# Kernel tuning notes

Measured on AMD Instinct MI355X. Metric: run time of the kernel, lower is better.

Reference implementation:

```python
import jax, jax.numpy as jnp
import numpy as np
from jax import lax

C = 64
EPS = 1e-6

def ln2d(x, w, b):
    # channel-wise LN over HxW per (n, c)
    mean = x.mean(axis=(2, 3), keepdims=True)
    var = ((x - mean) ** 2).mean(axis=(2, 3), keepdims=True)
    return (x - mean) / jnp.sqrt(var + EPS) * w + b

def pw(x, w, b):
    # 1x1 conv: w [O, I], b [O]
    return jnp.einsum('nihw,oi->nohw', x, w) + b[None, :, None, None]

def dwconv3(x, w, b):
    # depthwise 3x3, w [2C, 1, 3, 3]
    y = lax.conv_general_dilated(x, w, window_strides=(1, 1), padding='SAME',
                                 feature_group_count=x.shape[1],
                                 dimension_numbers=('NCHW', 'OIHW', 'NCHW'))
    return y + b[None, :, None, None]

def simple_gate(x):
    x1, x2 = jnp.split(x, 2, axis=1)
    return x1 * x2

def setup_inputs() -> dict:
    key = jax.random.key(0)
    ks = jax.random.split(key, 16)
    s = 0.05
    return {
        'x': jax.random.normal(ks[0], (8, C, 256, 256), jnp.float32),
        'ln1_w': jnp.ones((1, C, 1, 1), jnp.float32),
        'ln1_b': jnp.zeros((1, C, 1, 1), jnp.float32),
        'pw1_w': jax.random.normal(ks[1], (2 * C, C), jnp.float32) * s,
        'pw1_b': jnp.zeros((2 * C,), jnp.float32),
        'dw_w': jax.random.normal(ks[2], (2 * C, 1, 3, 3), jnp.float32) * s,
        'dw_b': jnp.zeros((2 * C,), jnp.float32),
        'sca_w': jax.random.normal(ks[3], (C, C), jnp.float32) * s,
        'sca_b': jnp.zeros((C,), jnp.float32),
        'pw2_w': jax.random.normal(ks[4], (C, C), jnp.float32) * s,
        'pw2_b': jnp.zeros((C,), jnp.float32),
        'ln2_w': jnp.ones((1, C, 1, 1), jnp.float32),
        'ln2_b': jnp.zeros((1, C, 1, 1), jnp.float32),
        'pw3_w': jax.random.normal(ks[5], (2 * C, C), jnp.float32) * s,
        'pw3_b': jnp.zeros((2 * C,), jnp.float32),
        'pw4_w': jax.random.normal(ks[6], (C, C), jnp.float32) * s,
        'pw4_b': jnp.zeros((C,), jnp.float32),
        'beta1': jax.random.normal(ks[7], (1, C, 1, 1), jnp.float32) * 0.1,
        'beta2': jax.random.normal(ks[8], (1, C, 1, 1), jnp.float32) * 0.1,
    }

def reference(x, ln1_w, ln1_b, pw1_w, pw1_b, dw_w, dw_b, sca_w, sca_b,
              pw2_w, pw2_b, ln2_w, ln2_b, pw3_w, pw3_b, pw4_w, pw4_b,
              beta1, beta2):
    y = ln2d(x, ln1_w, ln1_b)
    y = pw(y, pw1_w, pw1_b)
    y = dwconv3(y, dw_w, dw_b)
    y = simple_gate(y)
    # SCA: global avg pool -> 1x1 conv -> sigmoid scale
    s = y.mean(axis=(2, 3), keepdims=True)          # [N, C, 1, 1]
    w = jax.nn.sigmoid(pw(s, sca_w, sca_b))
    y = y * w
    y = pw(y, pw2_w, pw2_b)
    x = x + beta1 * y
    y2 = ln2d(x, ln2_w, ln2_b)
    y2 = pw(y2, pw3_w, pw3_b)
    y2 = simple_gate(y2)
    y2 = pw(y2, pw4_w, pw4_b)
    return x + beta2 * y2
```

## Files before the change

kernel.cpp:

```cpp
#include <hip/hip_runtime.h>
#include <hip/hip_bf16.h>

#define NB 8
#define CC 64
#define HWP 65536

typedef __attribute__((ext_vector_type(8))) short short8;
typedef __attribute__((ext_vector_type(4))) float f32x4;

__device__ __forceinline__ short f2bf(float f) {
  union { float f; unsigned u; } v; v.f = f;
  return (short)((v.u + 0x7FFF + ((v.u >> 16) & 1)) >> 16);
}
__device__ __forceinline__ float bf2f(unsigned short u) {
  union { unsigned u; float f; } v; v.u = ((unsigned)u) << 16; return v.f;
}

__global__ __launch_bounds__(256) void ln_stats_kernel(
    const float* __restrict__ x, const float* __restrict__ lw,
    const float* __restrict__ lb, float* __restrict__ a, float* __restrict__ b) {
  int plane = blockIdx.x;
  int c = plane & 63;
  const float4* p4 = (const float4*)(x + (size_t)plane * HWP);
  float s = 0.f, s2 = 0.f;
  for (int i = threadIdx.x; i < HWP / 4; i += 256) {
    float4 v = p4[i];
    s  += v.x + v.y + v.z + v.w;
    s2 += v.x * v.x + v.y * v.y + v.z * v.z + v.w * v.w;
  }
  for (int off = 32; off; off >>= 1) {
    s  += __shfl_down(s, off);
    s2 += __shfl_down(s2, off);
  }
  __shared__ float ls[4], ls2[4];
  int wid = threadIdx.x >> 6, lid = threadIdx.x & 63;
  if (lid == 0) { ls[wid] = s; ls2[wid] = s2; }
  __syncthreads();
  if (threadIdx.x == 0) {
    float S  = ls[0] + ls[1] + ls[2] + ls[3];
    float S2 = ls2[0] + ls2[1] + ls2[2] + ls2[3];
    float mean = S * (1.f / (float)HWP);
    float var  = S2 * (1.f / (float)HWP) - mean * mean;
    float rstd = rsqrtf(var + 1e-6f);
    float av = rstd * lw[c];
    a[plane] = av;
    b[plane] = lb[c] - mean * av;
  }
}

__global__ void fold_kernel(const float* __restrict__ w, const float* __restrict__ pb,
                            const float* __restrict__ a, const float* __restrict__ b,
                            float* __restrict__ wf, float* __restrict__ cf, int O) {
  int idx = blockIdx.x * blockDim.x + threadIdx.x;
  if (idx >= NB * O) return;
  int n = idx / O, o = idx - n * O;
  const float* an = a + n * 64;
  const float* bn = b + n * 64;
  const float* wo = w + o * 64;
  float* wfo = wf + (size_t)idx * 64;
  float cc = pb[o];
  for (int i = 0; i < 64; i++) { float wv = wo[i]; wfo[i] = wv * an[i]; cc += wv * bn[i]; }
  cf[idx] = cc;
}

__global__ __launch_bounds__(256, 2) void gemm_pw1_kernel(
    const float* __restrict__ x, const float* __restrict__ wf,
    const float* __restrict__ cf, unsigned short* __restrict__ z) {
  int n = blockIdx.y;
  int lane = threadIdx.x & 63, wid = threadIdx.x >> 6;
  int col = lane & 15, quad = lane >> 4;
  short8 a[8][2];
  const float* wfn = wf + (size_t)n * 128 * 64;
  #pragma unroll
  for (int mt = 0; mt < 8; mt++)
    #pragma unroll
    for (int ks = 0; ks < 2; ks++) {
      const float* wp = wfn + (mt * 16 + col) * 64 + ks * 32 + quad * 8;
      short8 v;
      #pragma unroll
      for (int j = 0; j < 8; j++) v[j] = f2bf(wp[j]);
      a[mt][ks] = v;
    }
  float cb[8][4];
  #pragma unroll
  for (int mt = 0; mt < 8; mt++)
    #pragma unroll
    for (int r = 0; r < 4; r++) cb[mt][r] = cf[n * 128 + mt * 16 + quad * 4 + r];
  const float* xn = x + (size_t)n * 64 * HWP;
  unsigned short* zn = z + (size_t)n * 128 * HWP;
  int pxbase = blockIdx.x * 256 + wid * 16 + col;

  auto load_b = [&](int p, short8* bf) {
    #pragma unroll
    for (int ks = 0; ks < 2; ks++) {
      short8 v;
      #pragma unroll
      for (int j = 0; j < 8; j++)
        v[j] = f2bf(xn[(size_t)(ks * 32 + quad * 8 + j) * HWP + p]);
      bf[ks] = v;
    }
  };

  short8 bb[2][2];
  load_b(pxbase, bb[0]);
  #pragma unroll
  for (int tile = 0; tile < 4; tile++) {
    int cur = tile & 1, nxt = cur ^ 1;
    int p = pxbase + tile * 64;
    if (tile < 3) load_b(p + 64, bb[nxt]);
    f32x4 acc[8];
    #pragma unroll
    for (int mt = 0; mt < 8; mt++) {
      acc[mt] = (f32x4){0.f, 0.f, 0.f, 0.f};
      acc[mt] = __builtin_amdgcn_mfma_f32_16x16x32_bf16(a[mt][0], bb[cur][0], acc[mt], 0, 0, 0);
      acc[mt] = __builtin_amdgcn_mfma_f32_16x16x32_bf16(a[mt][1], bb[cur][1], acc[mt], 0, 0, 0);
    }
    #pragma unroll
    for (int mt = 0; mt < 8; mt++)
      #pragma unroll
      for (int r = 0; r < 4; r++)
        zn[(size_t)(mt * 16 + quad * 4 + r) * HWP + p] =
            (unsigned short)f2bf(acc[mt][r] + cb[mt][r]);
  }
}

__global__ __launch_bounds__(256) void dwgate_kernel(
    const unsigned short* __restrict__ z, const float* __restrict__ dww,
    const float* __restrict__ dwb, unsigned short* __restrict__ t,
    float* __restrict__ pooled2) {
  int blk = blockIdx.x;
  int plane = blk >> 1, half = blk & 1;
  int n = plane >> 6, c = plane & 63;
  int lane = threadIdx.x & 63, wv = threadIdx.x >> 6;
  const unsigned short* z0 = z + ((size_t)n * 128 + c) * HWP;
  const unsigned short* z1 = z0 + (size_t)64 * HWP;
  unsigned short* tp = t + (size_t)plane * HWP;
  float w0[9], w1[9];
  #pragma unroll
  for (int k = 0; k < 9; k++) { w0[k] = dww[c * 9 + k]; w1[k] = dww[(c + 64) * 9 + k]; }
  float bias0 = dwb[c], bias1 = dwb[c + 64];
  int r0 = half * 128 + wv * 32;
  int colb = lane * 4;

  float fa[3][4], la[3], ra[3];
  float fb[3][4], lb_[3], rb[3];

  auto loadrow = [&](const unsigned short* base, int h, float* f, float& l, float& r) {
    if ((unsigned)h < 256u) {
      ushort4 u = *(const ushort4*)(base + h * 256 + colb);
      f[0] = bf2f(u.x); f[1] = bf2f(u.y); f[2] = bf2f(u.z); f[3] = bf2f(u.w);
    } else {
      f[0] = f[1] = f[2] = f[3] = 0.f;
    }
    float ll = __shfl_up(f[3], 1);
    float rr = __shfl_down(f[0], 1);
    l = (lane == 0) ? 0.f : ll;
    r = (lane == 63) ? 0.f : rr;
  };

  loadrow(z0, r0 - 1, fa[0], la[0], ra[0]);
  loadrow(z1, r0 - 1, fb[0], lb_[0], rb[0]);
  loadrow(z0, r0,     fa[1], la[1], ra[1]);
  loadrow(z1, r0,     fb[1], lb_[1], rb[1]);

  float lsum = 0.f;
  #pragma unroll 2
  for (int h = r0; h < r0 + 32; h++) {
    loadrow(z0, h + 1, fa[2], la[2], ra[2]);
    loadrow(z1, h + 1, fb[2], lb_[2], rb[2]);
    float o0[4] = {bias0, bias0, bias0, bias0};
    float o1[4] = {bias1, bias1, bias1, bias1};
    #pragma unroll
    for (int rr_ = 0; rr_ < 3; rr_++) {
      float wl0 = w0[rr_ * 3], wc0 = w0[rr_ * 3 + 1], wr0 = w0[rr_ * 3 + 2];
      float wl1 = w1[rr_ * 3], wc1 = w1[rr_ * 3 + 1], wr1 = w1[rr_ * 3 + 2];
      const float* f0 = fa[rr_]; const float* f1 = fb[rr_];
      float l0 = la[rr_], r0h = ra[rr_], l1 = lb_[rr_], r1h = rb[rr_];
      o0[0] += wl0 * l0    + wc0 * f0[0] + wr0 * f0[1];
      o0[1] += wl0 * f0[0] + wc0 * f0[1] + wr0 * f0[2];
      o0[2] += wl0 * f0[1] + wc0 * f0[2] + wr0 * f0[3];
      o0[3] += wl0 * f0[2] + wc0 * f0[3] + wr0 * r0h;
      o1[0] += wl1 * l1    + wc1 * f1[0] + wr1 * f1[1];
      o1[1] += wl1 * f1[0] + wc1 * f1[1] + wr1 * f1[2];
      o1[2] += wl1 * f1[1] + wc1 * f1[2] + wr1 * f1[3];
      o1[3] += wl1 * f1[2] + wc1 * f1[3] + wr1 * r1h;
    }
    float g0 = o0[0] * o1[0], g1 = o0[1] * o1[1];
    float g2 = o0[2] * o1[2], g3 = o0[3] * o1[3];
    uint2 pk;
    pk.x = (unsigned)(unsigned short)f2bf(g0) | ((unsigned)(unsigned short)f2bf(g1) << 16);
    pk.y = (unsigned)(unsigned short)f2bf(g2) | ((unsigned)(unsigned short)f2bf(g3) << 16);
    *(uint2*)(tp + (size_t)h * 256 + colb) = pk;
    lsum += (g0 + g1) + (g2 + g3);
    #pragma unroll
    for (int i = 0; i < 4; i++) { fa[0][i] = fa[1][i]; fa[1][i] = fa[2][i];
                                  fb[0][i] = fb[1][i]; fb[1][i] = fb[2][i]; }
    la[0] = la[1]; la[1] = la[2]; ra[0] = ra[1]; ra[1] = ra[2];
    lb_[0] = lb_[1]; lb_[1] = lb_[2]; rb[0] = rb[1]; rb[1] = rb[2];
  }
  for (int off = 32; off; off >>= 1) lsum += __shfl_down(lsum, off);
  __shared__ float ls[4];
  if (lane == 0) ls[wv] = lsum;
  __syncthreads();
  if (threadIdx.x == 0) pooled2[plane * 2 + half] = ls[0] + ls[1] + ls[2] + ls[3];
}

__global__ void sca_kernel(const float* __restrict__ pooled2, const float* __restrict__ sw,
                           const float* __restrict__ sb, float* __restrict__ sca) {
  int idx = blockIdx.x * blockDim.x + threadIdx.x;
  if (idx >= 512) return;
  int n = idx >> 6, o = idx & 63;
  float s = sb[o];
  const float* pm = pooled2 + n * 64 * 2;
  for (int i = 0; i < 64; i++)
    s += sw[o * 64 + i] * (pm[i * 2] + pm[i * 2 + 1]) * (1.f / 65536.f);
  sca[idx] = 1.f / (1.f + expf(-s));
}

__global__ void fold_pw2_kernel(const float* __restrict__ w, const float* __restrict__ pb,
                                const float* __restrict__ sca, const float* __restrict__ beta1,
                                float* __restrict__ wf, float* __restrict__ cf) {
  int idx = blockIdx.x * blockDim.x + threadIdx.x;
  if (idx >= 512) return;
  int n = idx >> 6, o = idx & 63;
  float bt = beta1[o];
  const float* sn = sca + n * 64;
  float* wfo = wf + (size_t)idx * 64;
  for (int i = 0; i < 64; i++) wfo[i] = bt * w[o * 64 + i] * sn[i];
  cf[idx] = bt * pb[o];
}

__global__ __launch_bounds__(256, 2) void gemm_pw2_kernel(
    const unsigned short* __restrict__ t, const float* __restrict__ x,
    const float* __restrict__ wf, const float* __restrict__ cf,
    float* __restrict__ x1, float* __restrict__ part_sum, float* __restrict__ part_sq) {
  __shared__ float red_s[4][64], red_q[4][64];
  int n = blockIdx.y;
  int lane = threadIdx.x & 63, wid = threadIdx.x >> 6;
  int col = lane & 15, quad = lane >> 4;
  short8 a[4][2];
  const float* wfn = wf + (size_t)n * 64 * 64;
  #pragma unroll
  for (int mt = 0; mt < 4; mt++)
    #pragma unroll
    for (int ks = 0; ks < 2; ks++) {
      const float* wp = wfn + (mt * 16 + col) * 64 + ks * 32 + quad * 8;
      short8 v;
      #pragma unroll
      for (int j = 0; j < 8; j++) v[j] = f2bf(wp[j]);
      a[mt][ks] = v;
    }
  float cb[4][4];
  #pragma unroll
  for (int mt = 0; mt < 4; mt++)
    #pragma unroll
    for (int r = 0; r < 4; r++) cb[mt][r] = cf[n * 64 + mt * 16 + quad * 4 + r];
  const unsigned short* tn = t + (size_t)n * 64 * HWP;
  const float* xn = x + (size_t)n * 64 * HWP;
  float* x1n = x1 + (size_t)n * 64 * HWP;
  int pxbase = blockIdx.x * 256 + wid * 16 + col;

  auto load_t = [&](int p, short8* bf) {
    #pragma unroll
    for (int ks = 0; ks < 2; ks++) {
      short8 v;
      #pragma unroll
      for (int j = 0; j < 8; j++)
        v[j] = (short)tn[(size_t)(ks * 32 + quad * 8 + j) * HWP + p];
      bf[ks] = v;
    }
  };
  auto load_x = [&](int p, float (*xv)[4]) {
    #pragma unroll
    for (int mt = 0; mt < 4; mt++)
      #pragma unroll
      for (int r = 0; r < 4; r++)
        xv[mt][r] = xn[(size_t)(mt * 16 + quad * 4 + r) * HWP + p];
  };

  float sacc[4][4], qacc[4][4];
  #pragma unroll
  for (int mt = 0; mt < 4; mt++)
    #pragma unroll
    for (int r = 0; r < 4; r++) { sacc[mt][r] = 0.f; qacc[mt][r] = 0.f; }

  short8 bb[2][2];
  float xv[2][4][4];
  load_t(pxbase, bb[0]);
  load_x(pxbase, xv[0]);
  #pragma unroll
  for (int tile = 0; tile < 4; tile++) {
    int cur = tile & 1, nxt = cur ^ 1;
    int p = pxbase + tile * 64;
    if (tile < 3) { load_t(p + 64, bb[nxt]); load_x(p + 64, xv[nxt]); }
    f32x4 acc[4];
    #pragma unroll
    for (int mt = 0; mt < 4; mt++) {
      acc[mt] = (f32x4){0.f, 0.f, 0.f, 0.f};
      acc[mt] = __builtin_amdgcn_mfma_f32_16x16x32_bf16(a[mt][0], bb[cur][0], acc[mt], 0, 0, 0);
      acc[mt] = __builtin_amdgcn_mfma_f32_16x16x32_bf16(a[mt][1], bb[cur][1], acc[mt], 0, 0, 0);
    }
    #pragma unroll
    for (int mt = 0; mt < 4; mt++)
      #pragma unroll
      for (int r = 0; r < 4; r++) {
        size_t idx = (size_t)(mt * 16 + quad * 4 + r) * HWP + p;
        float v = xv[cur][mt][r] + acc[mt][r] + cb[mt][r];
        x1n[idx] = v;
        sacc[mt][r] += v;
        qacc[mt][r] += v * v;
      }
  }
  #pragma unroll
  for (int mt = 0; mt < 4; mt++)
    #pragma unroll
    for (int r = 0; r < 4; r++) {
      float s = sacc[mt][r], q = qacc[mt][r];
      #pragma unroll
      for (int off = 1; off < 16; off <<= 1) {
        s += __shfl_xor(s, off);
        q += __shfl_xor(q, off);
      }
      if (col == 0) {
        int o = mt * 16 + quad * 4 + r;
        red_s[wid][o] = s; red_q[wid][o] = q;
      }
    }
  __syncthreads();
  if (threadIdx.x < 64) {
    int c = threadIdx.x;
    float s = red_s[0][c] + red_s[1][c] + red_s[2][c] + red_s[3][c];
    float q = red_q[0][c] + red_q[1][c] + red_q[2][c] + red_q[3][c];
    size_t pidx = ((size_t)n * 64 + c) * 256 + blockIdx.x;
    part_sum[pidx] = s;
    part_sq[pidx]  = q;
  }
}

__global__ __launch_bounds__(256) void ln2fold_kernel(
    const float* __restrict__ w, const float* __restrict__ pb,
    const float* __restrict__ ps, const float* __restrict__ pq,
    const float* __restrict__ lw, const float* __restrict__ lb,
    float* __restrict__ wf, float* __restrict__ cf) {
  __shared__ float aa[64], bb[64];
  int n = blockIdx.x;
  if (threadIdx.x < 64) {
    int c = threadIdx.x;
    const float* p1 = ps + ((size_t)n * 64 + c) * 256;
    const float* p2 = pq + ((size_t)n * 64 + c) * 256;
    float S = 0.f, S2 = 0.f;
    for (int k = 0; k < 256; k++) { S += p1[k]; S2 += p2[k]; }
    float mean = S * (1.f / (float)HWP);
    float var  = S2 * (1.f / (float)HWP) - mean * mean;
    float rstd = rsqrtf(var + 1e-6f);
    float av = rstd * lw[c];
    aa[c] = av;
    bb[c] = lb[c] - mean * av;
  }
  __syncthreads();
  if (threadIdx.x < 128) {
    int o = threadIdx.x;
    const float* wo = w + o * 64;
    float* wfo = wf + ((size_t)n * 128 + o) * 64;
    float cc = pb[o];
    for (int i = 0; i < 64; i++) { float wv = wo[i]; wfo[i] = wv * aa[i]; cc += wv * bb[i]; }
    cf[n * 128 + o] = cc;
  }
}

__global__ __launch_bounds__(256, 2) void final_mfma_kernel(
    const float* __restrict__ x1, const float* __restrict__ w3f,
    const float* __restrict__ c3f, const float* __restrict__ w4,
    const float* __restrict__ pb4, const float* __restrict__ beta2,
    float* __restrict__ out) {
  __shared__ float s_c3[128];
  __shared__ float s_b2[64];
  __shared__ float s_c4[64];
  __shared__ __align__(16) unsigned g_lds[64 * 33];
  int n = blockIdx.y;
  int lane = threadIdx.x & 63, wid = threadIdx.x >> 6;
  int col = lane & 15, quad = lane >> 4;
  if (threadIdx.x < 128) s_c3[threadIdx.x] = c3f[n * 128 + threadIdx.x];
  if (threadIdx.x < 64) { s_b2[threadIdx.x] = beta2[threadIdx.x]; s_c4[threadIdx.x] = pb4[threadIdx.x]; }
  short8 a3[8][2];
  const float* wfn = w3f + (size_t)n * 128 * 64;
  #pragma unroll
  for (int mt = 0; mt < 8; mt++)
    #pragma unroll
    for (int ks = 0; ks < 2; ks++) {
      const float* wp = wfn + (mt * 16 + col) * 64 + ks * 32 + quad * 8;
      short8 v;
      #pragma unroll
      for (int j = 0; j < 8; j++) v[j] = f2bf(wp[j]);
      a3[mt][ks] = v;
    }
  short8 a4[4][2];
  #pragma unroll
  for (int mt = 0; mt < 4; mt++)
    #pragma unroll
    for (int ks = 0; ks < 2; ks++) {
      const float* wp = w4 + (mt * 16 + col) * 64 + ks * 32 + quad * 8;
      short8 v;
      #pragma unroll
      for (int j = 0; j < 8; j++) v[j] = f2bf(wp[j]);
      a4[mt][ks] = v;
    }
  __syncthreads();
  const float* x1n = x1 + (size_t)n * 64 * HWP;
  float* outn = out + (size_t)n * 64 * HWP;
  int pxbase = blockIdx.x * 256 + wid * 16 + col;
  unsigned* grow = g_lds + (wid * 16 + col) * 33;

  auto load_b1 = [&](int p, short8* bf) {
    #pragma unroll
    for (int ks = 0; ks < 2; ks++) {
      short8 v;
      #pragma unroll
      for (int j = 0; j < 8; j++)
        v[j] = f2bf(x1n[(size_t)(ks * 32 + quad * 8 + j) * HWP + p]);
      bf[ks] = v;
    }
  };

  short8 bb1[2][2];
  load_b1(pxbase, bb1[0]);
  #pragma unroll
  for (int tile = 0; tile < 4; tile++) {
    int cur = tile & 1, nxt = cur ^ 1;
    int p = pxbase + tile * 64;
    if (tile < 3) load_b1(p + 64, bb1[nxt]);
    f32x4 acc[8];
    #pragma unroll
    for (int mt = 0; mt < 8; mt++) {
      acc[mt] = (f32x4){0.f, 0.f, 0.f, 0.f};
      acc[mt] = __builtin_amdgcn_mfma_f32_16x16x32_bf16(a3[mt][0], bb1[cur][0], acc[mt], 0, 0, 0);
      acc[mt] = __builtin_amdgcn_mfma_f32_16x16x32_bf16(a3[mt][1], bb1[cur][1], acc[mt], 0, 0, 0);
    }
    #pragma unroll
    for (int mt = 0; mt < 4; mt++)
      #pragma unroll
      for (int rr = 0; rr < 2; rr++) {
        int j0 = mt * 16 + quad * 4 + rr * 2;
        float ga = (acc[mt][rr * 2]     + s_c3[j0])     * (acc[mt + 4][rr * 2]     + s_c3[64 + j0]);
        float gb = (acc[mt][rr * 2 + 1] + s_c3[j0 + 1]) * (acc[mt + 4][rr * 2 + 1] + s_c3[64 + j0 + 1]);
        unsigned lo = (unsigned short)f2bf(ga);
        unsigned hi = (unsigned short)f2bf(gb);
        grow[j0 >> 1] = lo | (hi << 16);
      }
    __syncthreads();
    short8 b2[2];
    #pragma unroll
    for (int ks = 0; ks < 2; ks++)
      #pragma unroll
      for (int w = 0; w < 4; w++) {
        unsigned u = grow[ks * 16 + quad * 4 + w];
        b2[ks][2 * w]     = (short)(u & 0xFFFFu);
        b2[ks][2 * w + 1] = (short)(u >> 16);
      }
    __syncthreads();
    f32x4 acc2[4];
    #pragma unroll
    for (int mt = 0; mt < 4; mt++) {
      acc2[mt] = (f32x4){0.f, 0.f, 0.f, 0.f};
      acc2[mt] = __builtin_amdgcn_mfma_f32_16x16x32_bf16(a4[mt][0], b2[0], acc2[mt], 0, 0, 0);
      acc2[mt] = __builtin_amdgcn_mfma_f32_16x16x32_bf16(a4[mt][1], b2[1], acc2[mt], 0, 0, 0);
    }
    #pragma unroll
    for (int mt = 0; mt < 4; mt++)
      #pragma unroll
      for (int r = 0; r < 4; r++) {
        int o = mt * 16 + quad * 4 + r;
        size_t idx = (size_t)o * HWP + p;
        outn[idx] = x1n[idx] + s_b2[o] * (acc2[mt][r] + s_c4[o]);
      }
  }
}

extern "C" void kernel_launch(void* const* d_in, const int* in_sizes, int n_in,
                              void* d_out, int out_size, void* d_ws, size_t ws_size,
                              hipStream_t stream) {
  const float* x    = (const float*)d_in[0];
  const float* ln1w = (const float*)d_in[1];
  const float* ln1b = (const float*)d_in[2];
  const float* pw1w = (const float*)d_in[3];
  const float* pw1b = (const float*)d_in[4];
  const float* dww  = (const float*)d_in[5];
  const float* dwb  = (const float*)d_in[6];
  const float* scaw = (const float*)d_in[7];
  const float* scab = (const float*)d_in[8];
  const float* pw2w = (const float*)d_in[9];
  const float* pw2b = (const float*)d_in[10];
  const float* ln2w = (const float*)d_in[11];
  const float* ln2b = (const float*)d_in[12];
  const float* pw3w = (const float*)d_in[13];
  const float* pw3b = (const float*)d_in[14];
  const float* pw4w = (const float*)d_in[15];
  const float* pw4b = (const float*)d_in[16];
  const float* beta1= (const float*)d_in[17];
  const float* beta2= (const float*)d_in[18];
  float* out = (float*)d_out;

  char* ws = (char*)d_ws;
  unsigned short* z  = (unsigned short*)ws;
  float*          x1 = (float*)ws;
  unsigned short* t  = (unsigned short*)(ws + 134217728ull);
  float* sm = (float*)(ws + 134217728ull + 67108864ull);
  float* a1 = sm;               float* b1 = a1 + 512;
  float* w1f = b1 + 512;        float* c1f = w1f + 65536;
  float* pooled2 = c1f + 1024;  float* sca = pooled2 + 1024;
  float* w2f = sca + 512;       float* c2f = w2f + 32768;
  float* w3f = c2f + 512;       float* c3f = w3f + 65536;
  float* part_sum = (float*)d_out;
  float* part_sq  = part_sum + 131072;

  hipLaunchKernelGGL(ln_stats_kernel, dim3(512), dim3(256), 0, stream, x, ln1w, ln1b, a1, b1);
  hipLaunchKernelGGL(fold_kernel, dim3(4), dim3(256), 0, stream, pw1w, pw1b, a1, b1, w1f, c1f, 128);
  hipLaunchKernelGGL(gemm_pw1_kernel, dim3(256, 8), dim3(256), 0, stream, x, w1f, c1f, z);
  hipLaunchKernelGGL(dwgate_kernel, dim3(1024), dim3(256), 0, stream, z, dww, dwb, t, pooled2);
  hipLaunchKernelGGL(sca_kernel, dim3(2), dim3(256), 0, stream, pooled2, scaw, scab, sca);
  hipLaunchKernelGGL(fold_pw2_kernel, dim3(2), dim3(256), 0, stream, pw2w, pw2b, sca, beta1, w2f, c2f);
  hipLaunchKernelGGL(gemm_pw2_kernel, dim3(256, 8), dim3(256), 0, stream, t, x, w2f, c2f, x1,
                     part_sum, part_sq);
  hipLaunchKernelGGL(ln2fold_kernel, dim3(8), dim3(256), 0, stream,
                     pw3w, pw3b, part_sum, part_sq, ln2w, ln2b, w3f, c3f);
  hipLaunchKernelGGL(final_mfma_kernel, dim3(256, 8), dim3(256), 0, stream,
                     x1, w3f, c3f, pw4w, pw4b, beta2, out);
}
```

Before: 591.5 us.

## Pre-pack folded weights to bf16 MFMA layout, double grids, shuffle gate transpose

The fold kernels now write weights as bf16 already laid out in MFMA A-fragment order, so each GEMM kernel loads short8 vectors directly instead of converting fp32 per block. Bias is folded into the accumulator init, and pw4/beta2 are pre-folded in a new kernel. The grids of the pixel GEMMs and the depthwise kernel are doubled, giving each block half the pixels or rows. The final kernel replaces its LDS round-trip and two barriers with cross-lane shuffles. The LN stats kernel uses 512 threads, and the partial-sum buffers grow to match the larger grid.

```diff
diff --git a/kernel.cpp b/kernel.cpp
--- a/kernel.cpp
+++ b/kernel.cpp
@@ -2,7 +2,6 @@
 #include <hip/hip_bf16.h>
 
 #define NB 8
-#define CC 64
 #define HWP 65536
 
 typedef __attribute__((ext_vector_type(8))) short short8;
@@ -16,14 +15,14 @@
   union { unsigned u; float f; } v; v.u = ((unsigned)u) << 16; return v.f;
 }
 
-__global__ __launch_bounds__(256) void ln_stats_kernel(
+__global__ __launch_bounds__(512) void ln_stats_kernel(
     const float* __restrict__ x, const float* __restrict__ lw,
     const float* __restrict__ lb, float* __restrict__ a, float* __restrict__ b) {
   int plane = blockIdx.x;
   int c = plane & 63;
   const float4* p4 = (const float4*)(x + (size_t)plane * HWP);
   float s = 0.f, s2 = 0.f;
-  for (int i = threadIdx.x; i < HWP / 4; i += 256) {
+  for (int i = threadIdx.x; i < HWP / 4; i += 512) {
     float4 v = p4[i];
     s  += v.x + v.y + v.z + v.w;
     s2 += v.x * v.x + v.y * v.y + v.z * v.z + v.w * v.w;
@@ -32,13 +31,13 @@
     s  += __shfl_down(s, off);
     s2 += __shfl_down(s2, off);
   }
-  __shared__ float ls[4], ls2[4];
+  __shared__ float ls[8], ls2[8];
   int wid = threadIdx.x >> 6, lid = threadIdx.x & 63;
   if (lid == 0) { ls[wid] = s; ls2[wid] = s2; }
   __syncthreads();
   if (threadIdx.x == 0) {
-    float S  = ls[0] + ls[1] + ls[2] + ls[3];
-    float S2 = ls2[0] + ls2[1] + ls2[2] + ls2[3];
+    float S = 0.f, S2 = 0.f;
+    for (int k = 0; k < 8; k++) { S += ls[k]; S2 += ls2[k]; }
     float mean = S * (1.f / (float)HWP);
     float var  = S2 * (1.f / (float)HWP) - mean * mean;
     float rstd = rsqrtf(var + 1e-6f);
@@ -50,45 +49,47 @@
 
 __global__ void fold_kernel(const float* __restrict__ w, const float* __restrict__ pb,
                             const float* __restrict__ a, const float* __restrict__ b,
-                            float* __restrict__ wf, float* __restrict__ cf, int O) {
+                            unsigned short* __restrict__ wf16, float* __restrict__ cf, int O) {
   int idx = blockIdx.x * blockDim.x + threadIdx.x;
   if (idx >= NB * O) return;
   int n = idx / O, o = idx - n * O;
+  int MT = O >> 4;
   const float* an = a + n * 64;
   const float* bn = b + n * 64;
   const float* wo = w + o * 64;
-  float* wfo = wf + (size_t)idx * 64;
+  int mt = o >> 4, cl = o & 15;
   float cc = pb[o];
-  for (int i = 0; i < 64; i++) { float wv = wo[i]; wfo[i] = wv * an[i]; cc += wv * bn[i]; }
+  for (int i = 0; i < 64; i++) {
+    float wv = wo[i];
+    float wf = wv * an[i];
+    cc += wv * bn[i];
+    int ks = i >> 5, quad = (i >> 3) & 3, j = i & 7;
+    wf16[((((size_t)(n * MT + mt) * 2 + ks) * 16 + cl) * 4 + quad) * 8 + j] =
+        (unsigned short)f2bf(wf);
+  }
   cf[idx] = cc;
 }
 
 __global__ __launch_bounds__(256, 2) void gemm_pw1_kernel(
-    const float* __restrict__ x, const float* __restrict__ wf,
+    const float* __restrict__ x, const unsigned short* __restrict__ wf16,
     const float* __restrict__ cf, unsigned short* __restrict__ z) {
   int n = blockIdx.y;
   int lane = threadIdx.x & 63, wid = threadIdx.x >> 6;
   int col = lane & 15, quad = lane >> 4;
+  const short8* wv8 = (const short8*)wf16 + (size_t)n * 1024;
   short8 a[8][2];
-  const float* wfn = wf + (size_t)n * 128 * 64;
   #pragma unroll
   for (int mt = 0; mt < 8; mt++)
     #pragma unroll
-    for (int ks = 0; ks < 2; ks++) {
-      const float* wp = wfn + (mt * 16 + col) * 64 + ks * 32 + quad * 8;
-      short8 v;
-      #pragma unroll
-      for (int j = 0; j < 8; j++) v[j] = f2bf(wp[j]);
-      a[mt][ks] = v;
-    }
-  float cb[8][4];
+    for (int ks = 0; ks < 2; ks++)
+      a[mt][ks] = wv8[((mt * 2 + ks) * 16 + col) * 4 + quad];
+  f32x4 cb[8];
   #pragma unroll
   for (int mt = 0; mt < 8; mt++)
-    #pragma unroll
-    for (int r = 0; r < 4; r++) cb[mt][r] = cf[n * 128 + mt * 16 + quad * 4 + r];
+    cb[mt] = *(const f32x4*)(cf + n * 128 + mt * 16 + quad * 4);
   const float* xn = x + (size_t)n * 64 * HWP;
   unsigned short* zn = z + (size_t)n * 128 * HWP;
-  int pxbase = blockIdx.x * 256 + wid * 16 + col;
+  int pxbase = blockIdx.x * 128 + wid * 16 + col;
 
   auto load_b = [&](int p, short8* bf) {
     #pragma unroll
@@ -104,14 +105,14 @@
   short8 bb[2][2];
   load_b(pxbase, bb[0]);
   #pragma unroll
-  for (int tile = 0; tile < 4; tile++) {
+  for (int tile = 0; tile < 2; tile++) {
     int cur = tile & 1, nxt = cur ^ 1;
     int p = pxbase + tile * 64;
-    if (tile < 3) load_b(p + 64, bb[nxt]);
+    if (tile < 1) load_b(p + 64, bb[nxt]);
     f32x4 acc[8];
     #pragma unroll
     for (int mt = 0; mt < 8; mt++) {
-      acc[mt] = (f32x4){0.f, 0.f, 0.f, 0.f};
+      acc[mt] = cb[mt];
       acc[mt] = __builtin_amdgcn_mfma_f32_16x16x32_bf16(a[mt][0], bb[cur][0], acc[mt], 0, 0, 0);
       acc[mt] = __builtin_amdgcn_mfma_f32_16x16x32_bf16(a[mt][1], bb[cur][1], acc[mt], 0, 0, 0);
     }
@@ -120,16 +121,16 @@
       #pragma unroll
       for (int r = 0; r < 4; r++)
         zn[(size_t)(mt * 16 + quad * 4 + r) * HWP + p] =
-            (unsigned short)f2bf(acc[mt][r] + cb[mt][r]);
+            (unsigned short)f2bf(acc[mt][r]);
   }
 }
 
 __global__ __launch_bounds__(256) void dwgate_kernel(
     const unsigned short* __restrict__ z, const float* __restrict__ dww,
     const float* __restrict__ dwb, unsigned short* __restrict__ t,
-    float* __restrict__ pooled2) {
+    float* __restrict__ pooled4) {
   int blk = blockIdx.x;
-  int plane = blk >> 1, half = blk & 1;
+  int plane = blk >> 2, qtr = blk & 3;
   int n = plane >> 6, c = plane & 63;
   int lane = threadIdx.x & 63, wv = threadIdx.x >> 6;
   const unsigned short* z0 = z + ((size_t)n * 128 + c) * HWP;
@@ -139,7 +140,7 @@
   #pragma unroll
   for (int k = 0; k < 9; k++) { w0[k] = dww[c * 9 + k]; w1[k] = dww[(c + 64) * 9 + k]; }
   float bias0 = dwb[c], bias1 = dwb[c + 64];
-  int r0 = half * 128 + wv * 32;
+  int r0 = qtr * 64 + wv * 16;
   int colb = lane * 4;
 
   float fa[3][4], la[3], ra[3];
@@ -165,7 +166,7 @@
 
   float lsum = 0.f;
   #pragma unroll 2
-  for (int h = r0; h < r0 + 32; h++) {
+  for (int h = r0; h < r0 + 16; h++) {
     loadrow(z0, h + 1, fa[2], la[2], ra[2]);
     loadrow(z1, h + 1, fb[2], lb_[2], rb[2]);
     float o0[4] = {bias0, bias0, bias0, bias0};
@@ -202,63 +203,78 @@
   __shared__ float ls[4];
   if (lane == 0) ls[wv] = lsum;
   __syncthreads();
-  if (threadIdx.x == 0) pooled2[plane * 2 + half] = ls[0] + ls[1] + ls[2] + ls[3];
-}
-
-__global__ void sca_kernel(const float* __restrict__ pooled2, const float* __restrict__ sw,
+  if (threadIdx.x == 0) pooled4[plane * 4 + qtr] = ls[0] + ls[1] + ls[2] + ls[3];
+}
+
+__global__ void sca_kernel(const float* __restrict__ pooled4, const float* __restrict__ sw,
                            const float* __restrict__ sb, float* __restrict__ sca) {
   int idx = blockIdx.x * blockDim.x + threadIdx.x;
   if (idx >= 512) return;
   int n = idx >> 6, o = idx & 63;
   float s = sb[o];
-  const float* pm = pooled2 + n * 64 * 2;
+  const float* pm = pooled4 + n * 256;
   for (int i = 0; i < 64; i++)
-    s += sw[o * 64 + i] * (pm[i * 2] + pm[i * 2 + 1]) * (1.f / 65536.f);
+    s += sw[o * 64 + i] * (pm[i * 4] + pm[i * 4 + 1] + pm[i * 4 + 2] + pm[i * 4 + 3]) *
+         (1.f / 65536.f);
   sca[idx] = 1.f / (1.f + expf(-s));
 }
 
 __global__ void fold_pw2_kernel(const float* __restrict__ w, const float* __restrict__ pb,
                                 const float* __restrict__ sca, const float* __restrict__ beta1,
-                                float* __restrict__ wf, float* __restrict__ cf) {
+                                unsigned short* __restrict__ wf16, float* __restrict__ cf) {
   int idx = blockIdx.x * blockDim.x + threadIdx.x;
   if (idx >= 512) return;
   int n = idx >> 6, o = idx & 63;
   float bt = beta1[o];
   const float* sn = sca + n * 64;
-  float* wfo = wf + (size_t)idx * 64;
-  for (int i = 0; i < 64; i++) wfo[i] = bt * w[o * 64 + i] * sn[i];
+  int mt = o >> 4, cl = o & 15;
+  for (int i = 0; i < 64; i++) {
+    float wf = bt * w[o * 64 + i] * sn[i];
+    int ks = i >> 5, quad = (i >> 3) & 3, j = i & 7;
+    wf16[((((size_t)(n * 4 + mt) * 2 + ks) * 16 + cl) * 4 + quad) * 8 + j] =
+        (unsigned short)f2bf(wf);
+  }
   cf[idx] = bt * pb[o];
+}
+
+__global__ void fold4_kernel(const float* __restrict__ w4, const float* __restrict__ pb4,
+                             const float* __restrict__ beta2,
+                             unsigned short* __restrict__ wf16, float* __restrict__ cf) {
+  int o = threadIdx.x;
+  if (o >= 64) return;
+  float bt = beta2[o];
+  int mt = o >> 4, cl = o & 15;
+  for (int i = 0; i < 64; i++) {
+    int ks = i >> 5, quad = (i >> 3) & 3, j = i & 7;
+    wf16[((((size_t)mt * 2 + ks) * 16 + cl) * 4 + quad) * 8 + j] =
+        (unsigned short)f2bf(bt * w4[o * 64 + i]);
+  }
+  cf[o] = bt * pb4[o];
 }
 
 __global__ __launch_bounds__(256, 2) void gemm_pw2_kernel(
     const unsigned short* __restrict__ t, const float* __restrict__ x,
-    const float* __restrict__ wf, const float* __restrict__ cf,
+    const unsigned short* __restrict__ wf16, const float* __restrict__ cf,
     float* __restrict__ x1, float* __restrict__ part_sum, float* __restrict__ part_sq) {
   __shared__ float red_s[4][64], red_q[4][64];
   int n = blockIdx.y;
   int lane = threadIdx.x & 63, wid = threadIdx.x >> 6;
   int col = lane & 15, quad = lane >> 4;
+  const short8* wv8 = (const short8*)wf16 + (size_t)n * 512;
   short8 a[4][2];
-  const float* wfn = wf + (size_t)n * 64 * 64;
   #pragma unroll
   for (int mt = 0; mt < 4; mt++)
     #pragma unroll
-    for (int ks = 0; ks < 2; ks++) {
-      const float* wp = wfn + (mt * 16 + col) * 64 + ks * 32 + quad * 8;
-      short8 v;
-      #pragma unroll
-      for (int j = 0; j < 8; j++) v[j] = f2bf(wp[j]);
-      a[mt][ks] = v;
-    }
-  float cb[4][4];
+    for (int ks = 0; ks < 2; ks++)
+      a[mt][ks] = wv8[((mt * 2 + ks) * 16 + col) * 4 + quad];
+  f32x4 cb[4];
   #pragma unroll
   for (int mt = 0; mt < 4; mt++)
-    #pragma unroll
-    for (int r = 0; r < 4; r++) cb[mt][r] = cf[n * 64 + mt * 16 + quad * 4 + r];
+    cb[mt] = *(const f32x4*)(cf + n * 64 + mt * 16 + quad * 4);
   const unsigned short* tn = t + (size_t)n * 64 * HWP;
   const float* xn = x + (size_t)n * 64 * HWP;
   float* x1n = x1 + (size_t)n * 64 * HWP;
-  int pxbase = blockIdx.x * 256 + wid * 16 + col;
+  int pxbase = blockIdx.x * 128 + wid * 16 + col;
 
   auto load_t = [&](int p, short8* bf) {
     #pragma unroll
@@ -289,14 +305,14 @@
   load_t(pxbase, bb[0]);
   load_x(pxbase, xv[0]);
   #pragma unroll
-  for (int tile = 0; tile < 4; tile++) {
+  for (int tile = 0; tile < 2; tile++) {
     int cur = tile & 1, nxt = cur ^ 1;
     int p = pxbase + tile * 64;
-    if (tile < 3) { load_t(p + 64, bb[nxt]); load_x(p + 64, xv[nxt]); }
+    if (tile < 1) { load_t(p + 64, bb[nxt]); load_x(p + 64, xv[nxt]); }
     f32x4 acc[4];
     #pragma unroll
     for (int mt = 0; mt < 4; mt++) {
-      acc[mt] = (f32x4){0.f, 0.f, 0.f, 0.f};
+      acc[mt] = cb[mt];
       acc[mt] = __builtin_amdgcn_mfma_f32_16x16x32_bf16(a[mt][0], bb[cur][0], acc[mt], 0, 0, 0);
       acc[mt] = __builtin_amdgcn_mfma_f32_16x16x32_bf16(a[mt][1], bb[cur][1], acc[mt], 0, 0, 0);
     }
@@ -305,7 +321,7 @@
       #pragma unroll
       for (int r = 0; r < 4; r++) {
         size_t idx = (size_t)(mt * 16 + quad * 4 + r) * HWP + p;
-        float v = xv[cur][mt][r] + acc[mt][r] + cb[mt][r];
+        float v = xv[cur][mt][r] + acc[mt][r];
         x1n[idx] = v;
         sacc[mt][r] += v;
         qacc[mt][r] += v * v;
@@ -331,7 +347,7 @@
     int c = threadIdx.x;
     float s = red_s[0][c] + red_s[1][c] + red_s[2][c] + red_s[3][c];
     float q = red_q[0][c] + red_q[1][c] + red_q[2][c] + red_q[3][c];
-    size_t pidx = ((size_t)n * 64 + c) * 256 + blockIdx.x;
+    size_t pidx = ((size_t)n * 64 + c) * 512 + blockIdx.x;
     part_sum[pidx] = s;
     part_sq[pidx]  = q;
   }
@@ -341,75 +357,69 @@
     const float* __restrict__ w, const float* __restrict__ pb,
     const float* __restrict__ ps, const float* __restrict__ pq,
     const float* __restrict__ lw, const float* __restrict__ lb,
-    float* __restrict__ wf, float* __restrict__ cf) {
-  __shared__ float aa[64], bb[64];
+    unsigned short* __restrict__ wf16, float* __restrict__ cf) {
+  __shared__ float aa[64], bbv[64];
   int n = blockIdx.x;
   if (threadIdx.x < 64) {
     int c = threadIdx.x;
-    const float* p1 = ps + ((size_t)n * 64 + c) * 256;
-    const float* p2 = pq + ((size_t)n * 64 + c) * 256;
+    const float* p1 = ps + ((size_t)n * 64 + c) * 512;
+    const float* p2 = pq + ((size_t)n * 64 + c) * 512;
     float S = 0.f, S2 = 0.f;
-    for (int k = 0; k < 256; k++) { S += p1[k]; S2 += p2[k]; }
+    for (int k = 0; k < 512; k++) { S += p1[k]; S2 += p2[k]; }
     float mean = S * (1.f / (float)HWP);
     float var  = S2 * (1.f / (float)HWP) - mean * mean;
     float rstd = rsqrtf(var + 1e-6f);
     float av = rstd * lw[c];
     aa[c] = av;
-    bb[c] = lb[c] - mean * av;
+    bbv[c] = lb[c] - mean * av;
   }
   __syncthreads();
   if (threadIdx.x < 128) {
     int o = threadIdx.x;
     const float* wo = w + o * 64;
-    float* wfo = wf + ((size_t)n * 128 + o) * 64;
+    int mt = o >> 4, cl = o & 15;
     float cc = pb[o];
-    for (int i = 0; i < 64; i++) { float wv = wo[i]; wfo[i] = wv * aa[i]; cc += wv * bb[i]; }
+    for (int i = 0; i < 64; i++) {
+      float wv = wo[i];
+      float wf = wv * aa[i];
+      cc += wv * bbv[i];
+      int ks = i >> 5, quad = (i >> 3) & 3, j = i & 7;
+      wf16[((((size_t)(n * 8 + mt) * 2 + ks) * 16 + cl) * 4 + quad) * 8 + j] =
+          (unsigned short)f2bf(wf);
+    }
     cf[n * 128 + o] = cc;
   }
 }
 
 __global__ __launch_bounds__(256, 2) void final_mfma_kernel(
-    const float* __restrict__ x1, const float* __restrict__ w3f,
-    const float* __restrict__ c3f, const float* __restrict__ w4,
-    const float* __restrict__ pb4, const float* __restrict__ beta2,
-    float* __restrict__ out) {
+    const float* __restrict__ x1, const unsigned short* __restrict__ w3f16,
+    const float* __restrict__ c3f, const unsigned short* __restrict__ w4f16,
+    const float* __restrict__ c4f, float* __restrict__ out) {
   __shared__ float s_c3[128];
-  __shared__ float s_b2[64];
-  __shared__ float s_c4[64];
-  __shared__ __align__(16) unsigned g_lds[64 * 33];
+  __shared__ __align__(16) float s_c4[64];
   int n = blockIdx.y;
   int lane = threadIdx.x & 63, wid = threadIdx.x >> 6;
   int col = lane & 15, quad = lane >> 4;
   if (threadIdx.x < 128) s_c3[threadIdx.x] = c3f[n * 128 + threadIdx.x];
-  if (threadIdx.x < 64) { s_b2[threadIdx.x] = beta2[threadIdx.x]; s_c4[threadIdx.x] = pb4[threadIdx.x]; }
+  if (threadIdx.x < 64) s_c4[threadIdx.x] = c4f[threadIdx.x];
+  const short8* w3v = (const short8*)w3f16 + (size_t)n * 1024;
   short8 a3[8][2];
-  const float* wfn = w3f + (size_t)n * 128 * 64;
   #pragma unroll
   for (int mt = 0; mt < 8; mt++)
     #pragma unroll
-    for (int ks = 0; ks < 2; ks++) {
-      const float* wp = wfn + (mt * 16 + col) * 64 + ks * 32 + quad * 8;
-      short8 v;
-      #pragma unroll
-      for (int j = 0; j < 8; j++) v[j] = f2bf(wp[j]);
-      a3[mt][ks] = v;
-    }
+    for (int ks = 0; ks < 2; ks++)
+      a3[mt][ks] = w3v[((mt * 2 + ks) * 16 + col) * 4 + quad];
+  const short8* w4v = (const short8*)w4f16;
   short8 a4[4][2];
   #pragma unroll
   for (int mt = 0; mt < 4; mt++)
     #pragma unroll
-    for (int ks = 0; ks < 2; ks++) {
-      const float* wp = w4 + (mt * 16 + col) * 64 + ks * 32 + quad * 8;
-      short8 v;
-      #pragma unroll
-      for (int j = 0; j < 8; j++) v[j] = f2bf(wp[j]);
-      a4[mt][ks] = v;
-    }
+    for (int ks = 0; ks < 2; ks++)
+      a4[mt][ks] = w4v[((mt * 2 + ks) * 16 + col) * 4 + quad];
   __syncthreads();
   const float* x1n = x1 + (size_t)n * 64 * HWP;
   float* outn = out + (size_t)n * 64 * HWP;
-  int pxbase = blockIdx.x * 256 + wid * 16 + col;
-  unsigned* grow = g_lds + (wid * 16 + col) * 33;
+  int pxbase = blockIdx.x * 128 + wid * 16 + col;
 
   auto load_b1 = [&](int p, short8* bf) {
     #pragma unroll
@@ -425,10 +435,10 @@
   short8 bb1[2][2];
   load_b1(pxbase, bb1[0]);
   #pragma unroll
-  for (int tile = 0; tile < 4; tile++) {
+  for (int tile = 0; tile < 2; tile++) {
     int cur = tile & 1, nxt = cur ^ 1;
     int p = pxbase + tile * 64;
-    if (tile < 3) load_b1(p + 64, bb1[nxt]);
+    if (tile < 1) load_b1(p + 64, bb1[nxt]);
     f32x4 acc[8];
     #pragma unroll
     for (int mt = 0; mt < 8; mt++) {
@@ -436,42 +446,42 @@
       acc[mt] = __builtin_amdgcn_mfma_f32_16x16x32_bf16(a3[mt][0], bb1[cur][0], acc[mt], 0, 0, 0);
       acc[mt] = __builtin_amdgcn_mfma_f32_16x16x32_bf16(a3[mt][1], bb1[cur][1], acc[mt], 0, 0, 0);
     }
+    unsigned pd[4][2];
     #pragma unroll
     for (int mt = 0; mt < 4; mt++)
       #pragma unroll
-      for (int rr = 0; rr < 2; rr++) {
-        int j0 = mt * 16 + quad * 4 + rr * 2;
-        float ga = (acc[mt][rr * 2]     + s_c3[j0])     * (acc[mt + 4][rr * 2]     + s_c3[64 + j0]);
-        float gb = (acc[mt][rr * 2 + 1] + s_c3[j0 + 1]) * (acc[mt + 4][rr * 2 + 1] + s_c3[64 + j0 + 1]);
-        unsigned lo = (unsigned short)f2bf(ga);
-        unsigned hi = (unsigned short)f2bf(gb);
-        grow[j0 >> 1] = lo | (hi << 16);
+      for (int u = 0; u < 2; u++) {
+        int c0 = mt * 16 + quad * 4 + 2 * u;
+        float ga = (acc[mt][2 * u]     + s_c3[c0])     * (acc[mt + 4][2 * u]     + s_c3[64 + c0]);
+        float gb = (acc[mt][2 * u + 1] + s_c3[c0 + 1]) * (acc[mt + 4][2 * u + 1] + s_c3[64 + c0 + 1]);
+        pd[mt][u] = (unsigned)(unsigned short)f2bf(ga) |
+                    ((unsigned)(unsigned short)f2bf(gb) << 16);
       }
-    __syncthreads();
-    short8 b2[2];
+    short8 b2f[2];
     #pragma unroll
     for (int ks = 0; ks < 2; ks++)
       #pragma unroll
       for (int w = 0; w < 4; w++) {
-        unsigned u = grow[ks * 16 + quad * 4 + w];
-        b2[ks][2 * w]     = (short)(u & 0xFFFFu);
-        b2[ks][2 * w + 1] = (short)(u >> 16);
+        int src = ((quad & 1) * 2 + (w >> 1)) * 16 + col;
+        unsigned v0 = (unsigned)__shfl((int)pd[ks * 2][w & 1], src, 64);
+        unsigned v1 = (unsigned)__shfl((int)pd[ks * 2 + 1][w & 1], src, 64);
+        unsigned u = (quad & 2) ? v1 : v0;
+        b2f[ks][2 * w]     = (short)(u & 0xFFFFu);
+        b2f[ks][2 * w + 1] = (short)(u >> 16);
       }
-    __syncthreads();
     f32x4 acc2[4];
     #pragma unroll
     for (int mt = 0; mt < 4; mt++) {
-      acc2[mt] = (f32x4){0.f, 0.f, 0.f, 0.f};
-      acc2[mt] = __builtin_amdgcn_mfma_f32_16x16x32_bf16(a4[mt][0], b2[0], acc2[mt], 0, 0, 0);
-      acc2[mt] = __builtin_amdgcn_mfma_f32_16x16x32_bf16(a4[mt][1], b2[1], acc2[mt], 0, 0, 0);
+      acc2[mt] = *(const f32x4*)&s_c4[mt * 16 + quad * 4];
+      acc2[mt] = __builtin_amdgcn_mfma_f32_16x16x32_bf16(a4[mt][0], b2f[0], acc2[mt], 0, 0, 0);
+      acc2[mt] = __builtin_amdgcn_mfma_f32_16x16x32_bf16(a4[mt][1], b2f[1], acc2[mt], 0, 0, 0);
     }
     #pragma unroll
     for (int mt = 0; mt < 4; mt++)
       #pragma unroll
       for (int r = 0; r < 4; r++) {
-        int o = mt * 16 + quad * 4 + r;
-        size_t idx = (size_t)o * HWP + p;
-        outn[idx] = x1n[idx] + s_b2[o] * (acc2[mt][r] + s_c4[o]);
+        size_t idx = (size_t)(mt * 16 + quad * 4 + r) * HWP + p;
+        outn[idx] = x1n[idx] + acc2[mt][r];
       }
   }
 }
@@ -505,24 +515,32 @@
   float*          x1 = (float*)ws;
   unsigned short* t  = (unsigned short*)(ws + 134217728ull);
   float* sm = (float*)(ws + 134217728ull + 67108864ull);
-  float* a1 = sm;               float* b1 = a1 + 512;
-  float* w1f = b1 + 512;        float* c1f = w1f + 65536;
-  float* pooled2 = c1f + 1024;  float* sca = pooled2 + 1024;
-  float* w2f = sca + 512;       float* c2f = w2f + 32768;
-  float* w3f = c2f + 512;       float* c3f = w3f + 65536;
+  float* a1 = sm;
+  float* b1 = a1 + 512;
+  float* c1f = b1 + 512;
+  float* pooled4 = c1f + 1024;
+  float* sca = pooled4 + 2048;
+  float* c2f = sca + 512;
+  float* c3f = c2f + 512;
+  float* c4f = c3f + 1024;
+  unsigned short* w1f16 = (unsigned short*)(c4f + 64);
+  unsigned short* w2f16 = w1f16 + 65536;
+  unsigned short* w3f16 = w2f16 + 32768;
+  unsigned short* w4f16 = w3f16 + 65536;
   float* part_sum = (float*)d_out;
-  float* part_sq  = part_sum + 131072;
-
-  hipLaunchKernelGGL(ln_stats_kernel, dim3(512), dim3(256), 0, stream, x, ln1w, ln1b, a1, b1);
-  hipLaunchKernelGGL(fold_kernel, dim3(4), dim3(256), 0, stream, pw1w, pw1b, a1, b1, w1f, c1f, 128);
-  hipLaunchKernelGGL(gemm_pw1_kernel, dim3(256, 8), dim3(256), 0, stream, x, w1f, c1f, z);
-  hipLaunchKernelGGL(dwgate_kernel, dim3(1024), dim3(256), 0, stream, z, dww, dwb, t, pooled2);
-  hipLaunchKernelGGL(sca_kernel, dim3(2), dim3(256), 0, stream, pooled2, scaw, scab, sca);
-  hipLaunchKernelGGL(fold_pw2_kernel, dim3(2), dim3(256), 0, stream, pw2w, pw2b, sca, beta1, w2f, c2f);
-  hipLaunchKernelGGL(gemm_pw2_kernel, dim3(256, 8), dim3(256), 0, stream, t, x, w2f, c2f, x1,
+  float* part_sq  = part_sum + 262144;
+
+  hipLaunchKernelGGL(ln_stats_kernel, dim3(512), dim3(512), 0, stream, x, ln1w, ln1b, a1, b1);
+  hipLaunchKernelGGL(fold_kernel, dim3(4), dim3(256), 0, stream, pw1w, pw1b, a1, b1, w1f16, c1f, 128);
+  hipLaunchKernelGGL(fold4_kernel, dim3(1), dim3(64), 0, stream, pw4w, pw4b, beta2, w4f16, c4f);
+  hipLaunchKernelGGL(gemm_pw1_kernel, dim3(512, 8), dim3(256), 0, stream, x, w1f16, c1f, z);
+  hipLaunchKernelGGL(dwgate_kernel, dim3(2048), dim3(256), 0, stream, z, dww, dwb, t, pooled4);
+  hipLaunchKernelGGL(sca_kernel, dim3(2), dim3(256), 0, stream, pooled4, scaw, scab, sca);
+  hipLaunchKernelGGL(fold_pw2_kernel, dim3(2), dim3(256), 0, stream, pw2w, pw2b, sca, beta1, w2f16, c2f);
+  hipLaunchKernelGGL(gemm_pw2_kernel, dim3(512, 8), dim3(256), 0, stream, t, x, w2f16, c2f, x1,
                      part_sum, part_sq);
   hipLaunchKernelGGL(ln2fold_kernel, dim3(8), dim3(256), 0, stream,
-                     pw3w, pw3b, part_sum, part_sq, ln2w, ln2b, w3f, c3f);
-  hipLaunchKernelGGL(final_mfma_kernel, dim3(256, 8), dim3(256), 0, stream,
-                     x1, w3f, c3f, pw4w, pw4b, beta2, out);
-}
+                     pw3w, pw3b, part_sum, part_sq, ln2w, ln2b, w3f16, c3f);
+  hipLaunchKernelGGL(final_mfma_kernel, dim3(512, 8), dim3(256), 0, stream,
+                     x1, w3f16, c3f, w4f16, c4f, out);
+}
```

Result: faster. 563.6 us (-4.7%).
